# Performance work log

Measured on AMD Instinct MI355X. Metric: run time of the kernel, lower is better.

Reference implementation:

```python
import jax, jax.numpy as jnp
import numpy as np

B, N, DIM, H, DH = 8, 1024, 768, 12, 64
INNER = H * DH
SCALE = DH ** -0.5


def _bias_idx(n):
    # Reproduce the offset->id mapping from the torch __init__ loop:
    # offsets are first seen in row-major (p1, p2) order, so
    # id(0)=0, id(-k)=k (k=1..n-1), id(+k)=n-1+k.
    i = np.arange(n)[:, None]
    j = np.arange(n)[None, :]
    off = i - j
    idx = np.where(off <= 0, -off, n - 1 + off)
    return jnp.asarray(idx, dtype=jnp.int32)  # (n, n), values in [0, 2n-2]


def setup_inputs() -> dict:
    key = jax.random.key(0)
    ks = jax.random.split(key, 5)
    x = jax.random.normal(ks[0], (B, N, DIM), dtype=jnp.float32)
    w_qkv = jax.random.normal(ks[1], (DIM, 3 * INNER), dtype=jnp.float32) * (DIM ** -0.5)
    bias_table = jax.random.normal(ks[2], (H, 2 * N - 1), dtype=jnp.float32) * 0.02
    w_out = jax.random.normal(ks[3], (INNER, DIM), dtype=jnp.float32) * (INNER ** -0.5)
    b_out = jnp.zeros((DIM,), dtype=jnp.float32)
    bias_idx = _bias_idx(N)
    return {"x": x, "w_qkv": w_qkv, "bias_table": bias_table,
            "w_out": w_out, "b_out": b_out, "bias_idx": bias_idx}


def reference(x, w_qkv, bias_table, w_out, b_out, bias_idx):
    b, n, _ = x.shape
    qkv = x @ w_qkv  # (b, n, 3*inner)
    q, k, v = jnp.split(qkv, 3, axis=-1)
    def heads(t):
        return t.reshape(b, n, H, DH).transpose(0, 2, 1, 3)  # (b, h, n, d)
    q, k, v = heads(q), heads(k), heads(v)
    bias = bias_table[:, bias_idx]  # (h, n, n), gathered per-head relpos bias
    dots = jnp.einsum('bhid,bhjd->bhij', q, k) * SCALE + bias[None]
    attn = jax.nn.softmax(dots, axis=-1)
    out = jnp.einsum('bhij,bhjd->bhid', attn, v)
    out = out.transpose(0, 2, 1, 3).reshape(b, n, INNER)
    return out @ w_out + b_out
```

## Files before the change

kernel.cpp:

```cpp
#include <hip/hip_runtime.h>
#include <hip/hip_bf16.h>
#include <stdint.h>

typedef unsigned short u16;
typedef unsigned int u32;
typedef __bf16 bf16x8 __attribute__((ext_vector_type(8)));
typedef _Float16 f16x8 __attribute__((ext_vector_type(8)));
typedef _Float16 f16x2 __attribute__((ext_vector_type(2)));
typedef float f32x4 __attribute__((ext_vector_type(4)));
typedef unsigned short u16x4 __attribute__((ext_vector_type(4)));

#define SEQ     1024
#define DIM     768
#define NH      12
#define QKV_LD  2304
#define LOG2E   1.4426950408889634f
#define C1      0.18033688f

__device__ __forceinline__ float bf2f(u16 u) {
    union { unsigned v; float f; } x; x.v = ((unsigned)u) << 16; return x.f;
}
__device__ __forceinline__ u16 f2bf(float f) {
    union { float f; unsigned v; } x; x.f = f;
    unsigned r = (x.v + 0x7FFFu + ((x.v >> 16) & 1u)) >> 16;
    return (u16)r;
}
__device__ __forceinline__ void store_out(u16* p, float v)  { *p = f2bf(v); }
__device__ __forceinline__ void store_out(float* p, float v){ *p = v; }

__device__ __forceinline__ void async16(void* lds, const void* g) {
    __builtin_amdgcn_global_load_lds(
        (const __attribute__((address_space(1))) unsigned*)(uintptr_t)g,
        (__attribute__((address_space(3))) unsigned*)(unsigned)(uintptr_t)lds,
        16, 0, 0);
}

__device__ __forceinline__ int sw32(int row, int q) {
    return row * 32 + (q ^ ((row >> 1) & 3)) * 8;
}

__global__ __launch_bounds__(256) void cvt_k(const float* __restrict__ in,
                                             u16* __restrict__ out) {
    int i = (blockIdx.x * 256 + threadIdx.x) * 4;
    float4 v = *(const float4*)(in + i);
    u16x4 o = { f2bf(v.x), f2bf(v.y), f2bf(v.z), f2bf(v.w) };
    *(u16x4*)(out + i) = o;
}

__global__ __launch_bounds__(256) void transpose_k(const float* __restrict__ in,
                                                   u16* __restrict__ out,
                                                   int R, int C) {
    __shared__ __align__(16) float t[32][33];
    int c0 = blockIdx.x * 32, r0 = blockIdx.y * 32;
    int tx = threadIdx.x & 31, ty = threadIdx.x >> 5;
#pragma unroll
    for (int i = 0; i < 32; i += 8)
        t[ty + i][tx] = in[(size_t)(r0 + ty + i) * C + c0 + tx];
    __syncthreads();
#pragma unroll
    for (int i = 0; i < 32; i += 8)
        out[(size_t)(c0 + ty + i) * R + r0 + tx] = f2bf(t[tx][ty + i]);
}

__global__ __launch_bounds__(256) void vt_k(const u16* __restrict__ qkv,
                                            _Float16* __restrict__ vT) {
    __shared__ __align__(16) u16 t[32][33];
    int bh = blockIdx.z;
    int b = bh / 12, h = bh % 12;
    int key0 = blockIdx.x * 32, dh0 = blockIdx.y * 32;
    int tx = threadIdx.x & 31, ty = threadIdx.x >> 5;
#pragma unroll
    for (int i = 0; i < 32; i += 8)
        t[ty + i][tx] = qkv[(size_t)(b * SEQ + key0 + ty + i) * QKV_LD +
                            1536 + h * 64 + dh0 + tx];
    __syncthreads();
#pragma unroll
    for (int i = 0; i < 32; i += 8)
        vT[(size_t)(bh * 64 + dh0 + ty + i) * SEQ + key0 + tx] =
            (_Float16)bf2f(t[tx][ty + i]);
}

template <int HAS_BIAS, typename OUT_T>
__global__ __launch_bounds__(256) void gemm_bt(const u16* __restrict__ A,
                                               const u16* __restrict__ Bt,
                                               const float* __restrict__ bias,
                                               OUT_T* __restrict__ C,
                                               int M, int N, int K) {
    __shared__ __align__(16) u16 sA[128 * 32];
    __shared__ __align__(16) u16 sB[128 * 32];
    const int tid = threadIdx.x;
    const int lane = tid & 63;
    const int quad = lane >> 4, l16 = lane & 15;
    const int wave = tid >> 6;
    const int m0 = blockIdx.x * 128, n0 = blockIdx.y * 128;
    const int wm = (wave >> 1) * 64, wn = (wave & 1) * 64;

    f32x4 acc[4][4] = {};

    for (int k0 = 0; k0 < K; k0 += 32) {
        __syncthreads();
#pragma unroll
        for (int rep = 0; rep < 2; ++rep) {
            int i = rep * 256 + wave * 64 + lane;
            int row = i >> 2;
            int q = (i & 3) ^ ((row >> 1) & 3);
            async16(&sA[i * 8], A + (size_t)(m0 + row) * K + k0 + q * 8);
            async16(&sB[i * 8], Bt + (size_t)(n0 + row) * K + k0 + q * 8);
        }
        __syncthreads();

        bf16x8 af[4], bfr[4];
#pragma unroll
        for (int mi = 0; mi < 4; ++mi)
            af[mi] = *(const bf16x8*)&sA[sw32(wm + mi * 16 + l16, quad)];
#pragma unroll
        for (int nj = 0; nj < 4; ++nj)
            bfr[nj] = *(const bf16x8*)&sB[sw32(wn + nj * 16 + l16, quad)];
#pragma unroll
        for (int mi = 0; mi < 4; ++mi)
#pragma unroll
            for (int nj = 0; nj < 4; ++nj)
                acc[mi][nj] = __builtin_amdgcn_mfma_f32_16x16x32_bf16(
                    af[mi], bfr[nj], acc[mi][nj], 0, 0, 0);
    }

#pragma unroll
    for (int mi = 0; mi < 4; ++mi) {
#pragma unroll
        for (int nj = 0; nj < 4; ++nj) {
            int col = n0 + wn + nj * 16 + l16;
            float bv = HAS_BIAS ? bias[col] : 0.0f;
#pragma unroll
            for (int r = 0; r < 4; ++r) {
                int row = m0 + wm + mi * 16 + quad * 4 + r;
                store_out(&C[(size_t)row * N + col], acc[mi][nj][r] + bv);
            }
        }
    }
}

__global__ __launch_bounds__(256) void attn_k(const u16* __restrict__ qkv,
                                              const _Float16* __restrict__ vT,
                                              const float* __restrict__ bias_table,
                                              u16* __restrict__ out) {
    __shared__ __align__(16) u16 sK[2][64 * 64];
    __shared__ __align__(16) _Float16 sV[2][64 * 64];
    __shared__ __align__(16) u16 sBE[2048];
    __shared__ __align__(16) u16 sBO[2048];
    __shared__ __align__(16) _Float16 sP[4][32 * 64];

    const int tid = threadIdx.x;
    const int wave = tid >> 6, lane = tid & 63;
    const int quad = lane >> 4, l16 = lane & 15;
    const int bh = blockIdx.x;
    const int b = bh / NH, h = bh % NH;
    const int q0 = blockIdx.y * 128, wq = wave * 32;

    for (int i = tid; i < 2047; i += 256) {
        u16 v = f2bf(LOG2E * bias_table[h * 2047 + (i <= 1023 ? 1023 - i : i)]);
        sBE[i] = v;
        if (i >= 1) sBO[i - 1] = v;
    }

    bf16x8 qf[2][2];
#pragma unroll
    for (int nt = 0; nt < 2; ++nt)
#pragma unroll
        for (int hf = 0; hf < 2; ++hf)
            qf[nt][hf] = *(const bf16x8*)(qkv +
                (size_t)(b * SEQ + q0 + wq + nt * 16 + l16) * QKV_LD +
                h * 64 + hf * 32 + quad * 8);

    const u16* kg[2];
    const _Float16* vg[2];
    int lds_i[2];
#pragma unroll
    for (int rep = 0; rep < 2; ++rep) {
        int i = rep * 256 + wave * 64 + lane;
        int row = i >> 3;
        int c = (i & 7) ^ (row & 7);
        kg[rep] = qkv + (size_t)(b * SEQ + row) * QKV_LD + 768 + h * 64 + c * 8;
        vg[rep] = vT + (size_t)(bh * 64 + row) * SEQ + c * 8;
        lds_i[rep] = i * 8;
    }

    const int co0 = (quad ^ (l16 & 7)) * 8;
    const int co1 = co0 ^ 32;
    const int par = l16 & 1;
    const u32* blut = (const u32*)(par ? sBO : sBE);
    const int ib0 = q0 + wq + l16 - quad * 4 + 1020 - par;

#pragma unroll
    for (int rep = 0; rep < 2; ++rep) {
        async16(&sK[0][lds_i[rep]], kg[rep]);
        async16(&sV[0][lds_i[rep]], vg[rep]);
        kg[rep] += (size_t)64 * QKV_LD;
        vg[rep] += 64;
    }
    __syncthreads();

    f32x4 o[2][4] = {};
    f32x4 osum[2] = {};
    f16x8 ones;
#pragma unroll
    for (int z = 0; z < 8; ++z) ones[z] = (_Float16)1.0f;
    _Float16* sPw = sP[wave];

    for (int kt = 0; kt < SEQ / 64; ++kt) {
        const int cur = kt & 1;
        if (kt + 1 < SEQ / 64) {
            const int nxt = cur ^ 1;
#pragma unroll
            for (int rep = 0; rep < 2; ++rep) {
                async16(&sK[nxt][lds_i[rep]], kg[rep]);
                async16(&sV[nxt][lds_i[rep]], vg[rep]);
                kg[rep] += (size_t)64 * QKV_LD;
                vg[rep] += 64;
            }
        }
        const u16* sKc = sK[cur];
        const _Float16* sVc = sV[cur];
        const int ibk = ib0 - kt * 64;

#pragma unroll
        for (int mt = 0; mt < 4; ++mt) {
            const u16* kr = sKc + mt * 1024 + l16 * 64;
            bf16x8 af0 = *(const bf16x8*)(kr + co0);
            bf16x8 af1 = *(const bf16x8*)(kr + co1);
#pragma unroll
            for (int nt = 0; nt < 2; ++nt) {
                f32x4 s = {0.f, 0.f, 0.f, 0.f};
                s = __builtin_amdgcn_mfma_f32_16x16x32_bf16(af0, qf[nt][0], s, 0, 0, 0);
                s = __builtin_amdgcn_mfma_f32_16x16x32_bf16(af1, qf[nt][1], s, 0, 0, 0);
                int dw = (ibk + nt * 16 - mt * 16) >> 1;
                u32 d0 = blut[dw], d1 = blut[dw + 1];
                float bz[4];
                bz[3] = __uint_as_float(d0 << 16);
                bz[2] = __uint_as_float(d0 & 0xffff0000u);
                bz[1] = __uint_as_float(d1 << 16);
                bz[0] = __uint_as_float(d1 & 0xffff0000u);
                float p[4];
#pragma unroll
                for (int r = 0; r < 4; ++r)
                    p[r] = exp2f(fminf(s[r] * C1 + bz[r], 15.0f));
                f16x2 pk0 = __builtin_bit_cast(f16x2, __builtin_amdgcn_cvt_pkrtz(p[0], p[1]));
                f16x2 pk1 = __builtin_bit_cast(f16x2, __builtin_amdgcn_cvt_pkrtz(p[2], p[3]));
                int ch = (mt * 2 + (quad >> 1)) ^ (l16 & 7);
                _Float16* dst = &sPw[nt * 1024 + l16 * 64 + ch * 8 + (quad & 1) * 4];
                *(f16x2*)dst       = pk0;
                *(f16x2*)(dst + 2) = pk1;
            }
        }

        f16x8 pf[2][2];
#pragma unroll
        for (int mtp = 0; mtp < 2; ++mtp) {
            const _Float16* pr = sPw + mtp * 1024 + l16 * 64;
            pf[mtp][0] = *(const f16x8*)(pr + co0);
            pf[mtp][1] = *(const f16x8*)(pr + co1);
        }
#pragma unroll
        for (int mtp = 0; mtp < 2; ++mtp) {
            osum[mtp] = __builtin_amdgcn_mfma_f32_16x16x32_f16(pf[mtp][0], ones, osum[mtp], 0, 0, 0);
            osum[mtp] = __builtin_amdgcn_mfma_f32_16x16x32_f16(pf[mtp][1], ones, osum[mtp], 0, 0, 0);
        }
#pragma unroll
        for (int c4 = 0; c4 < 4; ++c4) {
            const _Float16* vr = sVc + c4 * 1024 + l16 * 64;
            f16x8 vf0 = *(const f16x8*)(vr + co0);
            f16x8 vf1 = *(const f16x8*)(vr + co1);
#pragma unroll
            for (int mtp = 0; mtp < 2; ++mtp) {
                o[mtp][c4] = __builtin_amdgcn_mfma_f32_16x16x32_f16(
                    pf[mtp][0], vf0, o[mtp][c4], 0, 0, 0);
                o[mtp][c4] = __builtin_amdgcn_mfma_f32_16x16x32_f16(
                    pf[mtp][1], vf1, o[mtp][c4], 0, 0, 0);
            }
        }
        __syncthreads();
    }

#pragma unroll
    for (int mtp = 0; mtp < 2; ++mtp) {
#pragma unroll
        for (int r = 0; r < 4; ++r) {
            float inv = __builtin_amdgcn_rcpf(osum[mtp][r]);
            int qrow = q0 + wq + mtp * 16 + quad * 4 + r;
#pragma unroll
            for (int c4 = 0; c4 < 4; ++c4)
                out[(size_t)(b * SEQ + qrow) * DIM + h * 64 + c4 * 16 + l16] =
                    f2bf(o[mtp][c4][r] * inv);
        }
    }
}

extern "C" void kernel_launch(void* const* d_in, const int* in_sizes, int n_in,
                              void* d_out, int out_size, void* d_ws, size_t ws_size,
                              hipStream_t stream) {
    const float* x          = (const float*)d_in[0];
    const float* w_qkv      = (const float*)d_in[1];
    const float* bias_table = (const float*)d_in[2];
    const float* w_out      = (const float*)d_in[3];
    const float* b_out      = (const float*)d_in[4];
    float* out = (float*)d_out;

    char* ws = (char*)d_ws;
    u16* ws_qkv        = (u16*)(ws);
    u16* ws_attn       = (u16*)(ws + 37748736);
    u16* ws_xb         = (u16*)(ws + 50331648);
    u16* ws_wqkvT      = (u16*)(ws + 62914560);
    u16* ws_woutT      = (u16*)(ws + 66453504);
    _Float16* ws_vT    = (_Float16*)(ws + 67633152);

    cvt_k<<<8 * 1024 * 768 / 1024, 256, 0, stream>>>(x, ws_xb);
    transpose_k<<<dim3(2304 / 32, 768 / 32), 256, 0, stream>>>(w_qkv, ws_wqkvT, 768, 2304);
    transpose_k<<<dim3(768 / 32, 768 / 32), 256, 0, stream>>>(w_out, ws_woutT, 768, 768);

    gemm_bt<0, u16><<<dim3(8192 / 128, 2304 / 128), 256, 0, stream>>>(
        ws_xb, ws_wqkvT, nullptr, ws_qkv, 8192, 2304, 768);

    vt_k<<<dim3(SEQ / 32, 2, 8 * NH), 256, 0, stream>>>(ws_qkv, ws_vT);

    attn_k<<<dim3(8 * NH, SEQ / 128, 1), 256, 0, stream>>>(ws_qkv, ws_vT, bias_table, ws_attn);

    gemm_bt<1, float><<<dim3(8192 / 128, 768 / 128), 256, 0, stream>>>(
        ws_attn, ws_woutT, b_out, out, 8192, 768, 768);
}
```

Measured before the change: 228.9 us.

## Double GEMM K-tile, merge bias LUTs with byte-permute, use raw exp2

The GEMM K step goes from 32 to 64 with an XOR-swizzled 128x64 LDS layout, which halves the number of barriers and loop iterations per tile at the cost of more LDS. The attention kernel drops the odd-shifted bias LUT copy and builds unaligned bias pairs with v_perm_b32 from three dword loads. exp2f is replaced by the hardware exp2 builtin to skip range handling. Together these aim to cut GEMM sync overhead and reduce LDS footprint and instruction count in the attention kernel.

```diff
diff --git a/kernel.cpp b/kernel.cpp
--- a/kernel.cpp
+++ b/kernel.cpp
@@ -35,10 +35,6 @@
         16, 0, 0);
 }
 
-__device__ __forceinline__ int sw32(int row, int q) {
-    return row * 32 + (q ^ ((row >> 1) & 3)) * 8;
-}
-
 __global__ __launch_bounds__(256) void cvt_k(const float* __restrict__ in,
                                              u16* __restrict__ out) {
     int i = (blockIdx.x * 256 + threadIdx.x) * 4;
@@ -86,8 +82,8 @@
                                                const float* __restrict__ bias,
                                                OUT_T* __restrict__ C,
                                                int M, int N, int K) {
-    __shared__ __align__(16) u16 sA[128 * 32];
-    __shared__ __align__(16) u16 sB[128 * 32];
+    __shared__ __align__(16) u16 sA[128 * 64];
+    __shared__ __align__(16) u16 sB[128 * 64];
     const int tid = threadIdx.x;
     const int lane = tid & 63;
     const int quad = lane >> 4, l16 = lane & 15;
@@ -95,33 +91,38 @@
     const int m0 = blockIdx.x * 128, n0 = blockIdx.y * 128;
     const int wm = (wave >> 1) * 64, wn = (wave & 1) * 64;
 
+    const int co0 = (quad ^ (l16 & 7)) * 8;
     f32x4 acc[4][4] = {};
 
-    for (int k0 = 0; k0 < K; k0 += 32) {
+    for (int k0 = 0; k0 < K; k0 += 64) {
         __syncthreads();
 #pragma unroll
-        for (int rep = 0; rep < 2; ++rep) {
-            int i = rep * 256 + wave * 64 + lane;
-            int row = i >> 2;
-            int q = (i & 3) ^ ((row >> 1) & 3);
-            async16(&sA[i * 8], A + (size_t)(m0 + row) * K + k0 + q * 8);
-            async16(&sB[i * 8], Bt + (size_t)(n0 + row) * K + k0 + q * 8);
+        for (int rep = 0; rep < 4; ++rep) {
+            int i = rep * 256 + tid;
+            int row = i >> 3;
+            int c = (i & 7) ^ (row & 7);
+            async16(&sA[i * 8], A + (size_t)(m0 + row) * K + k0 + c * 8);
+            async16(&sB[i * 8], Bt + (size_t)(n0 + row) * K + k0 + c * 8);
         }
         __syncthreads();
 
-        bf16x8 af[4], bfr[4];
-#pragma unroll
-        for (int mi = 0; mi < 4; ++mi)
-            af[mi] = *(const bf16x8*)&sA[sw32(wm + mi * 16 + l16, quad)];
-#pragma unroll
-        for (int nj = 0; nj < 4; ++nj)
-            bfr[nj] = *(const bf16x8*)&sB[sw32(wn + nj * 16 + l16, quad)];
-#pragma unroll
-        for (int mi = 0; mi < 4; ++mi)
+#pragma unroll
+        for (int ks = 0; ks < 2; ++ks) {
+            const int co = co0 ^ (ks * 32);
+            bf16x8 af[4], bfr[4];
+#pragma unroll
+            for (int mi = 0; mi < 4; ++mi)
+                af[mi] = *(const bf16x8*)&sA[(wm + mi * 16 + l16) * 64 + co];
 #pragma unroll
             for (int nj = 0; nj < 4; ++nj)
-                acc[mi][nj] = __builtin_amdgcn_mfma_f32_16x16x32_bf16(
-                    af[mi], bfr[nj], acc[mi][nj], 0, 0, 0);
+                bfr[nj] = *(const bf16x8*)&sB[(wn + nj * 16 + l16) * 64 + co];
+#pragma unroll
+            for (int mi = 0; mi < 4; ++mi)
+#pragma unroll
+                for (int nj = 0; nj < 4; ++nj)
+                    acc[mi][nj] = __builtin_amdgcn_mfma_f32_16x16x32_bf16(
+                        af[mi], bfr[nj], acc[mi][nj], 0, 0, 0);
+        }
     }
 
 #pragma unroll
@@ -146,7 +147,6 @@
     __shared__ __align__(16) u16 sK[2][64 * 64];
     __shared__ __align__(16) _Float16 sV[2][64 * 64];
     __shared__ __align__(16) u16 sBE[2048];
-    __shared__ __align__(16) u16 sBO[2048];
     __shared__ __align__(16) _Float16 sP[4][32 * 64];
 
     const int tid = threadIdx.x;
@@ -156,11 +156,8 @@
     const int b = bh / NH, h = bh % NH;
     const int q0 = blockIdx.y * 128, wq = wave * 32;
 
-    for (int i = tid; i < 2047; i += 256) {
-        u16 v = f2bf(LOG2E * bias_table[h * 2047 + (i <= 1023 ? 1023 - i : i)]);
-        sBE[i] = v;
-        if (i >= 1) sBO[i - 1] = v;
-    }
+    for (int i = tid; i < 2047; i += 256)
+        sBE[i] = f2bf(LOG2E * bias_table[h * 2047 + (i <= 1023 ? 1023 - i : i)]);
 
     bf16x8 qf[2][2];
 #pragma unroll
@@ -187,8 +184,12 @@
     const int co0 = (quad ^ (l16 & 7)) * 8;
     const int co1 = co0 ^ 32;
     const int par = l16 & 1;
-    const u32* blut = (const u32*)(par ? sBO : sBE);
     const int ib0 = q0 + wq + l16 - quad * 4 + 1020 - par;
+    const u32 sel3 = par ? 0x03020C0Cu : 0x01000C0Cu;
+    const u32 sel2 = par ? 0x05040C0Cu : 0x03020C0Cu;
+    const u32 sel1 = par ? 0x07060C0Cu : 0x05040C0Cu;
+    const u32 sel0 = par ? 0x05040C0Cu : 0x03020C0Cu;
+    const u32* lut32 = (const u32*)sBE;
 
 #pragma unroll
     for (int rep = 0; rep < 2; ++rep) {
@@ -232,17 +233,17 @@
                 f32x4 s = {0.f, 0.f, 0.f, 0.f};
                 s = __builtin_amdgcn_mfma_f32_16x16x32_bf16(af0, qf[nt][0], s, 0, 0, 0);
                 s = __builtin_amdgcn_mfma_f32_16x16x32_bf16(af1, qf[nt][1], s, 0, 0, 0);
-                int dw = (ibk + nt * 16 - mt * 16) >> 1;
-                u32 d0 = blut[dw], d1 = blut[dw + 1];
+                int w = (ibk + nt * 16 - mt * 16) >> 1;
+                u32 W0 = lut32[w], W1 = lut32[w + 1], W2 = lut32[w + 2];
                 float bz[4];
-                bz[3] = __uint_as_float(d0 << 16);
-                bz[2] = __uint_as_float(d0 & 0xffff0000u);
-                bz[1] = __uint_as_float(d1 << 16);
-                bz[0] = __uint_as_float(d1 & 0xffff0000u);
+                bz[3] = __uint_as_float(__builtin_amdgcn_perm(W1, W0, sel3));
+                bz[2] = __uint_as_float(__builtin_amdgcn_perm(W1, W0, sel2));
+                bz[1] = __uint_as_float(__builtin_amdgcn_perm(W1, W0, sel1));
+                bz[0] = __uint_as_float(__builtin_amdgcn_perm(W2, W1, sel0));
                 float p[4];
 #pragma unroll
                 for (int r = 0; r < 4; ++r)
-                    p[r] = exp2f(fminf(s[r] * C1 + bz[r], 15.0f));
+                    p[r] = __builtin_amdgcn_exp2f(fminf(s[r] * C1 + bz[r], 15.0f));
                 f16x2 pk0 = __builtin_bit_cast(f16x2, __builtin_amdgcn_cvt_pkrtz(p[0], p[1]));
                 f16x2 pk1 = __builtin_bit_cast(f16x2, __builtin_amdgcn_cvt_pkrtz(p[2], p[3]));
                 int ch = (mt * 2 + (quad >> 1)) ^ (l16 & 7);
```

Measured after the change: 198.4 us. 1.15x faster.
